# Kernel tuning notes

Hardware: AMD Instinct MI355X
Metric: run time of the kernel (lower is better)

The kernel has to match this reference:

```python
import jax, jax.numpy as jnp
import numpy as np

VOCAB, H, L, T = 50257, 1024, 2, 4096


def setup_inputs() -> dict:
    key = jax.random.key(0)
    ks = jax.random.split(key, 6)
    s = 1.0 / np.sqrt(H)  # torch GRU init scale
    return {
        "input_tensor": jax.random.randint(ks[0], (T,), 0, VOCAB, dtype=jnp.int64 if jax.config.jax_enable_x64 else jnp.int32),
        "embeddings": jax.random.normal(ks[1], (VOCAB, H), dtype=jnp.float32),
        "w_ih": jax.random.uniform(ks[2], (L, 3 * H, H), jnp.float32, -s, s),
        "w_hh": jax.random.uniform(ks[3], (L, 3 * H, H), jnp.float32, -s, s),
        "b_ih": jax.random.uniform(ks[4], (L, 3 * H), jnp.float32, -s, s),
        "b_hh": jax.random.uniform(ks[5], (L, 3 * H), jnp.float32, -s, s),
    }


def _gru_layer(x, wih, whh, bih, bhh):
    # x: [T, H]; returns outputs [T, H] and final hidden [H]
    gi = x @ wih.T + bih  # [T, 3H], input projections precomputed

    def step(h, gi_t):
        gh = h @ whh.T + bhh  # [3H]
        i_r, i_z, i_n = jnp.split(gi_t, 3)
        h_r, h_z, h_n = jnp.split(gh, 3)
        r = jax.nn.sigmoid(i_r + h_r)
        z = jax.nn.sigmoid(i_z + h_z)
        n = jnp.tanh(i_n + r * h_n)
        h_new = (1.0 - z) * n + z * h
        return h_new, h_new

    h0 = jnp.zeros((x.shape[-1],), x.dtype)
    h_fin, ys = jax.lax.scan(step, h0, gi)
    return ys, h_fin


def reference(input_tensor, embeddings, w_ih, w_hh, b_ih, b_hh):
    x = embeddings[input_tensor]  # [T, H] embedding lookup
    finals = []
    for l in range(w_ih.shape[0]):  # small fixed layer count
        x, h_fin = _gru_layer(x, w_ih[l], w_hh[l], b_ih[l], b_hh[l])
        finals.append(h_fin)
    encoder_outputs = x  # [T, H]
    encoder_hidden = jnp.stack(finals)[:, None, :]  # [L, 1, H]
    return encoder_outputs, encoder_hidden
```

## Files before the change

### kernel.cpp

```cpp
#include <hip/hip_runtime.h>
#include <hip/hip_bf16.h>


#define TT    4096
#define HDIM  1024
#define L0WG  64
#define L1WG  128
#define SBS   512
#define NREP  8
typedef unsigned long long u64;

__global__ void embed_kernel(const int* __restrict__ idx,
                             const float* __restrict__ emb,
                             float* __restrict__ x) {
    int t = blockIdx.x;
    int row = idx[t];
    const float4* src = reinterpret_cast<const float4*>(emb + (size_t)row * HDIM);
    float4* dst = reinterpret_cast<float4*>(x + (size_t)t * HDIM);
    dst[threadIdx.x] = src[threadIdx.x];
}

#define BM 64
#define BN 64
#define BK 32
__global__ __launch_bounds__(256)
void gemm_nt_bias(const float* __restrict__ A,
                  const float* __restrict__ Bw,
                  const float* __restrict__ bias,
                  float* __restrict__ C,
                  int M, int N, int K) {
    __shared__ float As[BK][BM];
    __shared__ float Bs[BK][BN];
    const int tid = threadIdx.x;
    const int m0 = blockIdx.x * BM;
    const int n0 = blockIdx.y * BN;
    const int tx = tid & 15, ty = tid >> 4;
    const int lr = tid >> 3;
    const int lc = (tid & 7) * 4;

    float acc[4][4] = {};

    for (int k0 = 0; k0 < K; k0 += BK) {
#pragma unroll
        for (int pass = 0; pass < 2; ++pass) {
            int m = lr + pass * 32;
            float4 v = *reinterpret_cast<const float4*>(A + (size_t)(m0 + m) * K + k0 + lc);
            As[lc + 0][m] = v.x; As[lc + 1][m] = v.y;
            As[lc + 2][m] = v.z; As[lc + 3][m] = v.w;
            float4 u = *reinterpret_cast<const float4*>(Bw + (size_t)(n0 + m) * K + k0 + lc);
            Bs[lc + 0][m] = u.x; Bs[lc + 1][m] = u.y;
            Bs[lc + 2][m] = u.z; Bs[lc + 3][m] = u.w;
        }
        __syncthreads();
#pragma unroll
        for (int kk = 0; kk < BK; ++kk) {
            float4 a = *reinterpret_cast<const float4*>(&As[kk][ty * 4]);
            float4 b = *reinterpret_cast<const float4*>(&Bs[kk][tx * 4]);
            float av[4] = {a.x, a.y, a.z, a.w};
            float bv[4] = {b.x, b.y, b.z, b.w};
#pragma unroll
            for (int i = 0; i < 4; ++i)
#pragma unroll
                for (int j = 0; j < 4; ++j)
                    acc[i][j] = fmaf(av[i], bv[j], acc[i][j]);
        }
        __syncthreads();
    }

    float4 b4 = *reinterpret_cast<const float4*>(bias + n0 + tx * 4);
    float bb[4] = {b4.x, b4.y, b4.z, b4.w};
#pragma unroll
    for (int i = 0; i < 4; ++i) {
        int m = m0 + ty * 4 + i;
        float4 o;
        o.x = acc[i][0] + bb[0];
        o.y = acc[i][1] + bb[1];
        o.z = acc[i][2] + bb[2];
        o.w = acc[i][3] + bb[3];
        *reinterpret_cast<float4*>(C + (size_t)m * N + n0 + tx * 4) = o;
    }
}

__device__ __forceinline__ float dot4(float4 a, float4 b) {
    return fmaf(a.x, b.x, fmaf(a.y, b.y, fmaf(a.z, b.z, a.w * b.w)));
}
__device__ __forceinline__ float fsig(float x) { return 1.f / (1.f + __expf(-x)); }
__device__ __forceinline__ float ftanh(float x) {
    return fmaf(-2.f, 1.f / (1.f + __expf(2.f * x)), 1.f);
}
__device__ __forceinline__ u64 pack_h(unsigned seq, float h) {
    return ((u64)seq << 32) | (u64)__float_as_uint(h);
}
__device__ __forceinline__ u64 aload(const u64* p) {
    return __hip_atomic_load(p, __ATOMIC_RELAXED, __HIP_MEMORY_SCOPE_AGENT);
}
__device__ __forceinline__ u64 poll_h(const u64* p, unsigned need) {
    u64 v = aload(p);
    while ((unsigned)(v >> 32) < need) v = aload(p);
    return v;
}
__device__ __forceinline__ void poll2(const u64* p0, const u64* p1, unsigned need,
                                      u64& v0, u64& v1) {
    v0 = aload(p0);
    v1 = aload(p1);
    while ((unsigned)(v0 >> 32) < need || (unsigned)(v1 >> 32) < need) {
        v0 = aload(p0);
        v1 = aload(p1);
    }
}
__device__ __forceinline__ void pub_h(u64* rep, int par, int idx, u64 v) {
#pragma unroll
    for (int r = 0; r < NREP; ++r)
        __hip_atomic_store(rep + ((size_t)r * 2 + par) * HDIM + idx, v,
                           __ATOMIC_RELAXED, __HIP_MEMORY_SCOPE_AGENT);
}
__device__ __forceinline__ void stage_y(const u64* lrow, unsigned need,
                                        float* lds_y, int l) {
    u64 v[16];
#pragma unroll
    for (int k = 0; k < 16; ++k) v[k] = aload(lrow + k * 64 + l);
#pragma unroll
    for (int k = 0; k < 16; ++k)
        while ((unsigned)(v[k] >> 32) < need) v[k] = aload(lrow + k * 64 + l);
#pragma unroll
    for (int k = 0; k < 16; ++k)
        lds_y[k * 64 + l] = __uint_as_float((unsigned)v[k]);
}

__global__ __launch_bounds__(SBS, 1)
void gru_pipe(const float* __restrict__ gi0,
              const float* __restrict__ whh0,
              const float* __restrict__ bhh0,
              const float* __restrict__ wih1,
              const float* __restrict__ whh1,
              const float* __restrict__ bih1,
              const float* __restrict__ bhh1,
              u64* y0log,
              float* __restrict__ out,
              u64* h0rep, u64* h1rep) {
    const int tid  = threadIdx.x;
    const int slot = tid >> 3;
    const int l8   = tid & 7;
    const int xcd  = blockIdx.x & 7;

    __shared__ float lds_h[HDIM];
    __shared__ float lds_y[HDIM];
    __shared__ float lds_gh[48];

    if (blockIdx.x < L0WG) {
        const int g = blockIdx.x;

        float4 Wlo[16], Whi[16];
        if (slot < 48) {
            const int q = slot >> 4, jl = slot & 15;
            const float4* row4 = reinterpret_cast<const float4*>(
                whh0 + (size_t)(q * HDIM + g * 16 + jl) * HDIM);
#pragma unroll
            for (int k4 = 0; k4 < 16; ++k4) Wlo[k4] = row4[k4 * 8 + l8];
#pragma unroll
            for (int k4 = 0; k4 < 16; ++k4) Whi[k4] = row4[(k4 + 16) * 8 + l8];
        } else {
#pragma unroll
            for (int k4 = 0; k4 < 16; ++k4) { Wlo[k4] = float4{0,0,0,0}; Whi[k4] = float4{0,0,0,0}; }
        }

        float bh0 = 0.f, bh1 = 0.f, bh2 = 0.f;
        float gir = 0.f, giz = 0.f, gin = 0.f;
        float h_own = 0.f;
        if (tid < 16) {
            const int gj = g * 16 + tid;
            bh0 = bhh0[0 * HDIM + gj];
            bh1 = bhh0[1 * HDIM + gj];
            bh2 = bhh0[2 * HDIM + gj];
            gir = gi0[gj];
            giz = gi0[HDIM + gj];
            gin = gi0[2 * HDIM + gj];
        }

        lds_h[tid] = 0.f;
        lds_h[tid + SBS] = 0.f;
        __syncthreads();

        const float4* lh4 = reinterpret_cast<const float4*>(lds_h);

        for (int t = 0; t < TT; ++t) {
            float nir = 0.f, niz = 0.f, nin = 0.f;
            if (tid < 16 && t + 1 < TT) {
                const float* base = gi0 + (size_t)(t + 1) * 3 * HDIM + g * 16 + tid;
                nir = base[0];
                niz = base[HDIM];
                nin = base[2 * HDIM];
            }

            if (slot < 48) {
                float p0 = 0.f, p1 = 0.f;
#pragma unroll
                for (int k4 = 0; k4 < 16; ++k4) p0 += dot4(Wlo[k4], lh4[k4 * 8 + l8]);
#pragma unroll
                for (int k4 = 0; k4 < 16; ++k4) p1 += dot4(Whi[k4], lh4[(k4 + 16) * 8 + l8]);
                float p = p0 + p1;
                p += __shfl_xor(p, 1);
                p += __shfl_xor(p, 2);
                p += __shfl_xor(p, 4);
                if (l8 == 0) lds_gh[slot] = p;
            }
            __syncthreads();

            if (tid < 16) {
                const int gj = g * 16 + tid;
                const float hr = lds_gh[tid]      + bh0;
                const float hz = lds_gh[16 + tid] + bh1;
                const float hn = lds_gh[32 + tid] + bh2;
                const float r = fsig(gir + hr);
                const float z = fsig(giz + hz);
                const float n = ftanh(gin + r * hn);
                const float h_new = (1.f - z) * n + z * h_own;
                h_own = h_new;
                const u64 pk = pack_h((unsigned)(t + 1), h_new);
                pub_h(h0rep, (t + 1) & 1, gj, pk);
                __hip_atomic_store(y0log + (size_t)t * HDIM + gj, pk,
                                   __ATOMIC_RELAXED, __HIP_MEMORY_SCOPE_AGENT);
                if (t == TT - 1) out[(size_t)TT * HDIM + gj] = h_new;
            }

            {
                const unsigned need = (unsigned)(t + 1);
                const u64* hp = h0rep + ((size_t)xcd * 2 + ((t + 1) & 1)) * HDIM;
                u64 v0, v1;
                poll2(hp + 2 * tid, hp + 2 * tid + 1, need, v0, v1);
                float2 hv;
                hv.x = __uint_as_float((unsigned)v0);
                hv.y = __uint_as_float((unsigned)v1);
                reinterpret_cast<float2*>(lds_h)[tid] = hv;
            }
            gir = nir; giz = niz; gin = nin;
            __syncthreads();
        }
    } else {
        const int g1 = blockIdx.x - L0WG;

        float4 Wlo[16], Whi[16];
        if (slot < 48) {
            const int ss = (slot < 24) ? slot : slot - 24;
            const int q = ss >> 3, jl = ss & 7;
            const float* mat = (slot < 24) ? whh1 : wih1;
            const float4* row4 = reinterpret_cast<const float4*>(
                mat + (size_t)(q * HDIM + g1 * 8 + jl) * HDIM);
#pragma unroll
            for (int k4 = 0; k4 < 16; ++k4) Wlo[k4] = row4[k4 * 8 + l8];
#pragma unroll
            for (int k4 = 0; k4 < 16; ++k4) Whi[k4] = row4[(k4 + 16) * 8 + l8];
        } else {
#pragma unroll
            for (int k4 = 0; k4 < 16; ++k4) { Wlo[k4] = float4{0,0,0,0}; Whi[k4] = float4{0,0,0,0}; }
        }

        float bh0 = 0.f, bh1 = 0.f, bh2 = 0.f;
        float bi0 = 0.f, bi1 = 0.f, bi2 = 0.f;
        float h_own = 0.f;
        if (tid < 8) {
            const int u = g1 * 8 + tid;
            bh0 = bhh1[0 * HDIM + u];
            bh1 = bhh1[1 * HDIM + u];
            bh2 = bhh1[2 * HDIM + u];
            bi0 = bih1[0 * HDIM + u];
            bi1 = bih1[1 * HDIM + u];
            bi2 = bih1[2 * HDIM + u];
        }

        lds_h[tid] = 0.f;
        lds_h[tid + SBS] = 0.f;
        if (tid >= 448) {
            stage_y(y0log, 1u, lds_y, tid - 448);
        }
        __syncthreads();

        const float4* lh4 = reinterpret_cast<const float4*>(lds_h);
        const float4* ly4 = reinterpret_cast<const float4*>(lds_y);

        for (int t = 0; t < TT; ++t) {
            if (slot < 48) {
                const float4* s4 = (slot < 24) ? lh4 : ly4;
                float p0 = 0.f, p1 = 0.f;
#pragma unroll
                for (int k4 = 0; k4 < 16; ++k4) p0 += dot4(Wlo[k4], s4[k4 * 8 + l8]);
#pragma unroll
                for (int k4 = 0; k4 < 16; ++k4) p1 += dot4(Whi[k4], s4[(k4 + 16) * 8 + l8]);
                float p = p0 + p1;
                p += __shfl_xor(p, 1);
                p += __shfl_xor(p, 2);
                p += __shfl_xor(p, 4);
                if (l8 == 0) lds_gh[slot] = p;
            }
            __syncthreads();

            if (tid < 8) {
                const int u = g1 * 8 + tid;
                const float hr = lds_gh[tid]      + bh0;
                const float hz = lds_gh[8 + tid]  + bh1;
                const float hn = lds_gh[16 + tid] + bh2;
                const float ir = lds_gh[24 + tid] + bi0;
                const float iz = lds_gh[32 + tid] + bi1;
                const float in_ = lds_gh[40 + tid] + bi2;
                const float r = fsig(ir + hr);
                const float z = fsig(iz + hz);
                const float n = ftanh(in_ + r * hn);
                const float h_new = (1.f - z) * n + z * h_own;
                h_own = h_new;
                pub_h(h1rep, (t + 1) & 1, u, pack_h((unsigned)(t + 1), h_new));
                out[(size_t)t * HDIM + u] = h_new;
                if (t == TT - 1) out[(size_t)TT * HDIM + HDIM + u] = h_new;
            }

            if (tid >= 448 && t + 1 < TT) {
                stage_y(y0log + (size_t)(t + 1) * HDIM, (unsigned)(t + 2),
                        lds_y, tid - 448);
            }

            {
                const unsigned need = (unsigned)(t + 1);
                const u64* hp = h1rep + ((size_t)xcd * 2 + ((t + 1) & 1)) * HDIM;
                u64 v0, v1;
                poll2(hp + 2 * tid, hp + 2 * tid + 1, need, v0, v1);
                float2 hv;
                hv.x = __uint_as_float((unsigned)v0);
                hv.y = __uint_as_float((unsigned)v1);
                reinterpret_cast<float2*>(lds_h)[tid] = hv;
            }
            __syncthreads();
        }
    }
}

extern "C" void kernel_launch(void* const* d_in, const int* in_sizes, int n_in,
                              void* d_out, int out_size, void* d_ws, size_t ws_size,
                              hipStream_t stream) {
    const int*   idx = (const int*)d_in[0];
    const float* emb = (const float*)d_in[1];
    const float* wih = (const float*)d_in[2];
    const float* whh = (const float*)d_in[3];
    const float* bih = (const float*)d_in[4];
    const float* bhh = (const float*)d_in[5];
    float* out = (float*)d_out;

    float* x     = (float*)d_ws;
    float* gi    = x  + (size_t)TT * HDIM;
    u64*   y0log = (u64*)(gi + (size_t)TT * 3 * HDIM);
    u64*   h0rep = y0log + (size_t)TT * HDIM;
    u64*   h1rep = h0rep + (size_t)NREP * 2 * HDIM;
    size_t zero_bytes = ((size_t)TT * HDIM + 2 * (size_t)NREP * 2 * HDIM) * 8;

    hipMemsetAsync(y0log, 0, zero_bytes, stream);

    embed_kernel<<<TT, 256, 0, stream>>>(idx, emb, x);

    const size_t wstride = (size_t)3 * HDIM * HDIM;
    const size_t bstride = (size_t)3 * HDIM;

    gemm_nt_bias<<<dim3(TT / BM, 3 * HDIM / BN), 256, 0, stream>>>(
        x, wih, bih, gi, TT, 3 * HDIM, HDIM);

    gru_pipe<<<L0WG + L1WG, SBS, 0, stream>>>(
        gi, whh, bhh,
        wih + wstride, whh + wstride, bih + bstride, bhh + bstride,
        y0log, out, h0rep, h1rep);
}
```

Baseline: 10.10 ms.

## Halve layer-1 workgroups, stage W_ih1 in LDS as bf16, prefetch y0 ahead

Layer 1 now runs on 64 workgroups of 16 hidden units each instead of 128 of 8. W_hh1 stays in registers, while this block's W_ih1 rows are converted to bf16 and kept in LDS. The input projection for step t+1 is computed from a double-buffered y0 row during the wait for the recurrent h broadcast, and waves 6-7 prefetch y0 two steps ahead. The intent is to shrink the set of participants in the per-step h1 exchange and take the input GEMV off the critical path. In exchange it adds bf16 rounding error on the input weights, about 96KB of LDS use, and a startup wait until layer 0 is LAG steps ahead.

```diff
diff --git a/kernel.cpp b/kernel.cpp
--- a/kernel.cpp
+++ b/kernel.cpp
@@ -5,9 +5,11 @@
 #define TT    4096
 #define HDIM  1024
 #define L0WG  64
-#define L1WG  128
+#define L1WG  64
 #define SBS   512
 #define NREP  8
+#define LAG   8
+typedef unsigned short ushort_t;
 typedef unsigned long long u64;
 
 __global__ void embed_kernel(const int* __restrict__ idx,
@@ -88,6 +90,12 @@
 __device__ __forceinline__ float ftanh(float x) {
     return fmaf(-2.f, 1.f / (1.f + __expf(2.f * x)), 1.f);
 }
+__device__ __forceinline__ float bflo(unsigned u) { return __uint_as_float(u << 16); }
+__device__ __forceinline__ float bfhi(unsigned u) { return __uint_as_float(u & 0xffff0000u); }
+__device__ __forceinline__ ushort_t f2bf(float f) {
+    unsigned u = __float_as_uint(f);
+    return (ushort_t)((u + 0x7FFFu + ((u >> 16) & 1u)) >> 16);
+}
 __device__ __forceinline__ u64 pack_h(unsigned seq, float h) {
     return ((u64)seq << 32) | (u64)__float_as_uint(h);
 }
@@ -114,17 +122,18 @@
         __hip_atomic_store(rep + ((size_t)r * 2 + par) * HDIM + idx, v,
                            __ATOMIC_RELAXED, __HIP_MEMORY_SCOPE_AGENT);
 }
-__device__ __forceinline__ void stage_y(const u64* lrow, unsigned need,
-                                        float* lds_y, int l) {
-    u64 v[16];
-#pragma unroll
-    for (int k = 0; k < 16; ++k) v[k] = aload(lrow + k * 64 + l);
-#pragma unroll
-    for (int k = 0; k < 16; ++k)
-        while ((unsigned)(v[k] >> 32) < need) v[k] = aload(lrow + k * 64 + l);
-#pragma unroll
-    for (int k = 0; k < 16; ++k)
-        lds_y[k * 64 + l] = __uint_as_float((unsigned)v[k]);
+__device__ __forceinline__ float dot_bf16(uint2 w0, uint2 w1, uint2 w2, uint2 w3,
+                                          float4 yA, float4 yB, float4 yC, float4 yD) {
+    float p = 0.f;
+    p = fmaf(bflo(w0.x), yA.x, p); p = fmaf(bfhi(w0.x), yA.y, p);
+    p = fmaf(bflo(w0.y), yA.z, p); p = fmaf(bfhi(w0.y), yA.w, p);
+    p = fmaf(bflo(w1.x), yB.x, p); p = fmaf(bfhi(w1.x), yB.y, p);
+    p = fmaf(bflo(w1.y), yB.z, p); p = fmaf(bfhi(w1.y), yB.w, p);
+    p = fmaf(bflo(w2.x), yC.x, p); p = fmaf(bfhi(w2.x), yC.y, p);
+    p = fmaf(bflo(w2.y), yC.z, p); p = fmaf(bfhi(w2.y), yC.w, p);
+    p = fmaf(bflo(w3.x), yD.x, p); p = fmaf(bfhi(w3.x), yD.y, p);
+    p = fmaf(bflo(w3.y), yD.z, p); p = fmaf(bfhi(w3.y), yD.w, p);
+    return p;
 }
 
 __global__ __launch_bounds__(SBS, 1)
@@ -141,11 +150,15 @@
     const int tid  = threadIdx.x;
     const int slot = tid >> 3;
     const int l8   = tid & 7;
+    const int wv   = tid >> 6;
+    const int ln   = tid & 63;
     const int xcd  = blockIdx.x & 7;
 
-    __shared__ float lds_h[HDIM];
-    __shared__ float lds_y[HDIM];
+    __shared__ __align__(16) ushort_t lds_wi[48 * HDIM];
+    __shared__ __align__(16) float lds_h[HDIM];
+    __shared__ __align__(16) float lds_y[2][HDIM];
     __shared__ float lds_gh[48];
+    __shared__ float lds_gi[2][48];
 
     if (blockIdx.x < L0WG) {
         const int g = blockIdx.x;
@@ -238,14 +251,13 @@
         }
     } else {
         const int g1 = blockIdx.x - L0WG;
+        const int u0 = g1 * 16;
 
         float4 Wlo[16], Whi[16];
         if (slot < 48) {
-            const int ss = (slot < 24) ? slot : slot - 24;
-            const int q = ss >> 3, jl = ss & 7;
-            const float* mat = (slot < 24) ? whh1 : wih1;
+            const int q = slot >> 4, jl = slot & 15;
             const float4* row4 = reinterpret_cast<const float4*>(
-                mat + (size_t)(q * HDIM + g1 * 8 + jl) * HDIM);
+                whh1 + (size_t)(q * HDIM + u0 + jl) * HDIM);
 #pragma unroll
             for (int k4 = 0; k4 < 16; ++k4) Wlo[k4] = row4[k4 * 8 + l8];
 #pragma unroll
@@ -255,56 +267,95 @@
             for (int k4 = 0; k4 < 16; ++k4) { Wlo[k4] = float4{0,0,0,0}; Whi[k4] = float4{0,0,0,0}; }
         }
 
-        float bh0 = 0.f, bh1 = 0.f, bh2 = 0.f;
-        float bi0 = 0.f, bi1 = 0.f, bi2 = 0.f;
+        for (int i = tid; i < 48 * 512; i += SBS) {
+            const int r = i >> 9, c = i & 511;
+            const size_t grow = (size_t)((r >> 4) * HDIM + u0 + (r & 15)) * HDIM;
+            const float2 a = *reinterpret_cast<const float2*>(wih1 + grow + 2 * c);
+            reinterpret_cast<unsigned*>(lds_wi)[r * 512 + c] =
+                (unsigned)f2bf(a.x) | ((unsigned)f2bf(a.y) << 16);
+        }
+
+        float bir = 0.f, biz = 0.f, bin = 0.f;
+        float bhr = 0.f, bhz = 0.f, bhn = 0.f;
         float h_own = 0.f;
-        if (tid < 8) {
-            const int u = g1 * 8 + tid;
-            bh0 = bhh1[0 * HDIM + u];
-            bh1 = bhh1[1 * HDIM + u];
-            bh2 = bhh1[2 * HDIM + u];
-            bi0 = bih1[0 * HDIM + u];
-            bi1 = bih1[1 * HDIM + u];
-            bi2 = bih1[2 * HDIM + u];
+        if (tid < 16) {
+            const int u = u0 + tid;
+            bir = bih1[u]; biz = bih1[HDIM + u]; bin = bih1[2 * HDIM + u];
+            bhr = bhh1[u]; bhz = bhh1[HDIM + u]; bhn = bhh1[2 * HDIM + u];
         }
 
         lds_h[tid] = 0.f;
         lds_h[tid + SBS] = 0.f;
-        if (tid >= 448) {
-            stage_y(y0log, 1u, lds_y, tid - 448);
+
+        if (tid == 0) (void)poll_h(y0log + (size_t)(LAG - 1) * HDIM, (unsigned)LAG);
+        __syncthreads();
+
+#pragma unroll
+        for (int s = 0; s < 2; ++s)
+#pragma unroll
+            for (int k = 0; k < 2; ++k) {
+                u64 v = poll_h(y0log + (size_t)s * HDIM + k * 512 + tid, (unsigned)(s + 1));
+                lds_y[s][k * 512 + tid] = __uint_as_float((unsigned)v);
+            }
+        __syncthreads();
+
+        if (wv < 6) {
+            const float4* ly4 = reinterpret_cast<const float4*>(lds_y[0]);
+            float4 yA = ly4[ln], yB = ly4[64 + ln], yC = ly4[128 + ln], yD = ly4[192 + ln];
+            const uint2* wi2 = reinterpret_cast<const uint2*>(lds_wi);
+#pragma unroll
+            for (int rr = 0; rr < 8; ++rr) {
+                const int row = wv * 8 + rr;
+                const uint2* wr = wi2 + row * 256;
+                float p = dot_bf16(wr[ln], wr[64 + ln], wr[128 + ln], wr[192 + ln],
+                                   yA, yB, yC, yD);
+                p += __shfl_xor(p, 1);  p += __shfl_xor(p, 2);
+                p += __shfl_xor(p, 4);  p += __shfl_xor(p, 8);
+                p += __shfl_xor(p, 16); p += __shfl_xor(p, 32);
+                if (ln == 0) lds_gi[0][row] = p;
+            }
         }
         __syncthreads();
 
         const float4* lh4 = reinterpret_cast<const float4*>(lds_h);
-        const float4* ly4 = reinterpret_cast<const float4*>(lds_y);
 
         for (int t = 0; t < TT; ++t) {
             if (slot < 48) {
-                const float4* s4 = (slot < 24) ? lh4 : ly4;
                 float p0 = 0.f, p1 = 0.f;
 #pragma unroll
-                for (int k4 = 0; k4 < 16; ++k4) p0 += dot4(Wlo[k4], s4[k4 * 8 + l8]);
-#pragma unroll
-                for (int k4 = 0; k4 < 16; ++k4) p1 += dot4(Whi[k4], s4[(k4 + 16) * 8 + l8]);
+                for (int k4 = 0; k4 < 16; ++k4) p0 += dot4(Wlo[k4], lh4[k4 * 8 + l8]);
+#pragma unroll
+                for (int k4 = 0; k4 < 16; ++k4) p1 += dot4(Whi[k4], lh4[(k4 + 16) * 8 + l8]);
                 float p = p0 + p1;
                 p += __shfl_xor(p, 1);
                 p += __shfl_xor(p, 2);
                 p += __shfl_xor(p, 4);
                 if (l8 == 0) lds_gh[slot] = p;
+            } else if (wv >= 6) {
+                const int s = t + 2;
+                if (s < TT) {
+                    const int tl = tid - 384;
+                    const u64* lr = y0log + (size_t)s * HDIM;
+                    u64 v[8];
+#pragma unroll
+                    for (int k = 0; k < 8; ++k) v[k] = aload(lr + k * 128 + tl);
+#pragma unroll
+                    for (int k = 0; k < 8; ++k)
+                        while ((unsigned)(v[k] >> 32) < (unsigned)(s + 1))
+                            v[k] = aload(lr + k * 128 + tl);
+#pragma unroll
+                    for (int k = 0; k < 8; ++k)
+                        lds_y[s & 1][k * 128 + tl] = __uint_as_float((unsigned)v[k]);
+                }
             }
             __syncthreads();
 
-            if (tid < 8) {
-                const int u = g1 * 8 + tid;
-                const float hr = lds_gh[tid]      + bh0;
-                const float hz = lds_gh[8 + tid]  + bh1;
-                const float hn = lds_gh[16 + tid] + bh2;
-                const float ir = lds_gh[24 + tid] + bi0;
-                const float iz = lds_gh[32 + tid] + bi1;
-                const float in_ = lds_gh[40 + tid] + bi2;
-                const float r = fsig(ir + hr);
-                const float z = fsig(iz + hz);
-                const float n = ftanh(in_ + r * hn);
+            if (tid < 16) {
+                const int u = u0 + tid;
+                const float r = fsig(lds_gi[t & 1][tid]      + bir + lds_gh[tid]      + bhr);
+                const float z = fsig(lds_gi[t & 1][16 + tid] + biz + lds_gh[16 + tid] + bhz);
+                const float n = ftanh(lds_gi[t & 1][32 + tid] + bin
+                                      + r * (lds_gh[32 + tid] + bhn));
                 const float h_new = (1.f - z) * n + z * h_own;
                 h_own = h_new;
                 pub_h(h1rep, (t + 1) & 1, u, pack_h((unsigned)(t + 1), h_new));
@@ -312,12 +363,24 @@
                 if (t == TT - 1) out[(size_t)TT * HDIM + HDIM + u] = h_new;
             }
 
-            if (tid >= 448 && t + 1 < TT) {
-                stage_y(y0log + (size_t)(t + 1) * HDIM, (unsigned)(t + 2),
-                        lds_y, tid - 448);
-            }
-
-            {
+            if (wv < 6 && t + 1 < TT) {
+                const float4* ly4 = reinterpret_cast<const float4*>(lds_y[(t + 1) & 1]);
+                float4 yA = ly4[ln], yB = ly4[64 + ln], yC = ly4[128 + ln], yD = ly4[192 + ln];
+                const uint2* wi2 = reinterpret_cast<const uint2*>(lds_wi);
+#pragma unroll
+                for (int rr = 0; rr < 8; ++rr) {
+                    const int row = wv * 8 + rr;
+                    const uint2* wr = wi2 + row * 256;
+                    float p = dot_bf16(wr[ln], wr[64 + ln], wr[128 + ln], wr[192 + ln],
+                                       yA, yB, yC, yD);
+                    p += __shfl_xor(p, 1);  p += __shfl_xor(p, 2);
+                    p += __shfl_xor(p, 4);  p += __shfl_xor(p, 8);
+                    p += __shfl_xor(p, 16); p += __shfl_xor(p, 32);
+                    if (ln == 0) lds_gi[(t + 1) & 1][row] = p;
+                }
+            }
+
+            if (t + 1 < TT) {
                 const unsigned need = (unsigned)(t + 1);
                 const u64* hp = h1rep + ((size_t)xcd * 2 + ((t + 1) & 1)) * HDIM;
                 u64 v0, v1;
```

New measurement: 16.34 ms. +61.8%, slower.

## Restructure GRU recurrence: per-wave row ownership, double-buffered LDS, one barrier per step

Applied to the files above, without the earlier changes.

Each wavefront (or half-wavefront in layer 0) now owns one hidden unit and computes all three gate dot products itself, reducing them with xor shuffles. This removes the LDS gate-partial exchange and one of the two block barriers per timestep. The h and y staging buffers are double-buffered so the single remaining barrier is enough. All threads now poll layer-0 outputs together with the layer-1 hidden state, replacing the dedicated staging waves. Publishing threads raise wave priority around the stores. The trade-off is more shuffle work and higher register pressure for the weight fragments held in every wave.

```diff
diff --git a/kernel.cpp b/kernel.cpp
--- a/kernel.cpp
+++ b/kernel.cpp
@@ -94,11 +94,6 @@
 __device__ __forceinline__ u64 aload(const u64* p) {
     return __hip_atomic_load(p, __ATOMIC_RELAXED, __HIP_MEMORY_SCOPE_AGENT);
 }
-__device__ __forceinline__ u64 poll_h(const u64* p, unsigned need) {
-    u64 v = aload(p);
-    while ((unsigned)(v >> 32) < need) v = aload(p);
-    return v;
-}
 __device__ __forceinline__ void poll2(const u64* p0, const u64* p1, unsigned need,
                                       u64& v0, u64& v1) {
     v0 = aload(p0);
@@ -108,23 +103,20 @@
         v1 = aload(p1);
     }
 }
+__device__ __forceinline__ void poll4(const u64* p0, const u64* p1, unsigned needh,
+                                      const u64* p2, const u64* p3, unsigned needy,
+                                      u64& v0, u64& v1, u64& v2, u64& v3) {
+    v0 = aload(p0); v1 = aload(p1); v2 = aload(p2); v3 = aload(p3);
+    while ((unsigned)(v0 >> 32) < needh || (unsigned)(v1 >> 32) < needh ||
+           (unsigned)(v2 >> 32) < needy || (unsigned)(v3 >> 32) < needy) {
+        v0 = aload(p0); v1 = aload(p1); v2 = aload(p2); v3 = aload(p3);
+    }
+}
 __device__ __forceinline__ void pub_h(u64* rep, int par, int idx, u64 v) {
 #pragma unroll
     for (int r = 0; r < NREP; ++r)
         __hip_atomic_store(rep + ((size_t)r * 2 + par) * HDIM + idx, v,
                            __ATOMIC_RELAXED, __HIP_MEMORY_SCOPE_AGENT);
-}
-__device__ __forceinline__ void stage_y(const u64* lrow, unsigned need,
-                                        float* lds_y, int l) {
-    u64 v[16];
-#pragma unroll
-    for (int k = 0; k < 16; ++k) v[k] = aload(lrow + k * 64 + l);
-#pragma unroll
-    for (int k = 0; k < 16; ++k)
-        while ((unsigned)(v[k] >> 32) < need) v[k] = aload(lrow + k * 64 + l);
-#pragma unroll
-    for (int k = 0; k < 16; ++k)
-        lds_y[k * 64 + l] = __uint_as_float((unsigned)v[k]);
 }
 
 __global__ __launch_bounds__(SBS, 1)
@@ -138,92 +130,76 @@
               u64* y0log,
               float* __restrict__ out,
               u64* h0rep, u64* h1rep) {
-    const int tid  = threadIdx.x;
-    const int slot = tid >> 3;
-    const int l8   = tid & 7;
-    const int xcd  = blockIdx.x & 7;
-
-    __shared__ float lds_h[HDIM];
-    __shared__ float lds_y[HDIM];
-    __shared__ float lds_gh[48];
+    const int tid = threadIdx.x;
+    const int xcd = blockIdx.x & 7;
+
+    __shared__ __align__(16) float lds_h[2][HDIM];
+    __shared__ __align__(16) float lds_y[2][HDIM];
 
     if (blockIdx.x < L0WG) {
         const int g = blockIdx.x;
-
-        float4 Wlo[16], Whi[16];
-        if (slot < 48) {
-            const int q = slot >> 4, jl = slot & 15;
-            const float4* row4 = reinterpret_cast<const float4*>(
-                whh0 + (size_t)(q * HDIM + g * 16 + jl) * HDIM);
-#pragma unroll
-            for (int k4 = 0; k4 < 16; ++k4) Wlo[k4] = row4[k4 * 8 + l8];
-#pragma unroll
-            for (int k4 = 0; k4 < 16; ++k4) Whi[k4] = row4[(k4 + 16) * 8 + l8];
-        } else {
-#pragma unroll
-            for (int k4 = 0; k4 < 16; ++k4) { Wlo[k4] = float4{0,0,0,0}; Whi[k4] = float4{0,0,0,0}; }
+        const int l = tid & 31;
+        const int u = g * 16 + (tid >> 5);
+
+        const float4* r0 = reinterpret_cast<const float4*>(whh0 + (size_t)(0 * HDIM + u) * HDIM);
+        const float4* r1 = reinterpret_cast<const float4*>(whh0 + (size_t)(1 * HDIM + u) * HDIM);
+        const float4* r2 = reinterpret_cast<const float4*>(whh0 + (size_t)(2 * HDIM + u) * HDIM);
+        float4 W0[8], W1[8], W2[8];
+#pragma unroll
+        for (int m = 0; m < 8; ++m) {
+            W0[m] = r0[m * 32 + l];
+            W1[m] = r1[m * 32 + l];
+            W2[m] = r2[m * 32 + l];
         }
 
         float bh0 = 0.f, bh1 = 0.f, bh2 = 0.f;
         float gir = 0.f, giz = 0.f, gin = 0.f;
         float h_own = 0.f;
-        if (tid < 16) {
-            const int gj = g * 16 + tid;
-            bh0 = bhh0[0 * HDIM + gj];
-            bh1 = bhh0[1 * HDIM + gj];
-            bh2 = bhh0[2 * HDIM + gj];
-            gir = gi0[gj];
-            giz = gi0[HDIM + gj];
-            gin = gi0[2 * HDIM + gj];
-        }
-
-        lds_h[tid] = 0.f;
-        lds_h[tid + SBS] = 0.f;
+        if (l == 0) {
+            bh0 = bhh0[u]; bh1 = bhh0[HDIM + u]; bh2 = bhh0[2 * HDIM + u];
+            gir = gi0[u];  giz = gi0[HDIM + u];  gin = gi0[2 * HDIM + u];
+        }
+
+        reinterpret_cast<float2*>(lds_h[0])[tid] = float2{0.f, 0.f};
         __syncthreads();
 
-        const float4* lh4 = reinterpret_cast<const float4*>(lds_h);
-
         for (int t = 0; t < TT; ++t) {
-            float nir = 0.f, niz = 0.f, nin = 0.f;
-            if (tid < 16 && t + 1 < TT) {
-                const float* base = gi0 + (size_t)(t + 1) * 3 * HDIM + g * 16 + tid;
-                nir = base[0];
-                niz = base[HDIM];
-                nin = base[2 * HDIM];
-            }
-
-            if (slot < 48) {
-                float p0 = 0.f, p1 = 0.f;
-#pragma unroll
-                for (int k4 = 0; k4 < 16; ++k4) p0 += dot4(Wlo[k4], lh4[k4 * 8 + l8]);
-#pragma unroll
-                for (int k4 = 0; k4 < 16; ++k4) p1 += dot4(Whi[k4], lh4[(k4 + 16) * 8 + l8]);
-                float p = p0 + p1;
-                p += __shfl_xor(p, 1);
-                p += __shfl_xor(p, 2);
-                p += __shfl_xor(p, 4);
-                if (l8 == 0) lds_gh[slot] = p;
-            }
-            __syncthreads();
-
-            if (tid < 16) {
-                const int gj = g * 16 + tid;
-                const float hr = lds_gh[tid]      + bh0;
-                const float hz = lds_gh[16 + tid] + bh1;
-                const float hn = lds_gh[32 + tid] + bh2;
-                const float r = fsig(gir + hr);
-                const float z = fsig(giz + hz);
-                const float n = ftanh(gin + r * hn);
+            const float4* lh4 = reinterpret_cast<const float4*>(lds_h[t & 1]);
+            float p0 = 0.f, p1 = 0.f, p2 = 0.f;
+#pragma unroll
+            for (int m = 0; m < 8; ++m) {
+                const float4 h4 = lh4[m * 32 + l];
+                p0 += dot4(W0[m], h4);
+                p1 += dot4(W1[m], h4);
+                p2 += dot4(W2[m], h4);
+            }
+#pragma unroll
+            for (int o = 1; o < 32; o <<= 1) {
+                p0 += __shfl_xor(p0, o);
+                p1 += __shfl_xor(p1, o);
+                p2 += __shfl_xor(p2, o);
+            }
+
+            if (l == 0) {
+                __builtin_amdgcn_s_setprio(1);
+                const float r = fsig(gir + p0 + bh0);
+                const float z = fsig(giz + p1 + bh1);
+                const float n = ftanh(gin + r * (p2 + bh2));
                 const float h_new = (1.f - z) * n + z * h_own;
                 h_own = h_new;
                 const u64 pk = pack_h((unsigned)(t + 1), h_new);
-                pub_h(h0rep, (t + 1) & 1, gj, pk);
-                __hip_atomic_store(y0log + (size_t)t * HDIM + gj, pk,
+                pub_h(h0rep, (t + 1) & 1, u, pk);
+                __hip_atomic_store(y0log + (size_t)t * HDIM + u, pk,
                                    __ATOMIC_RELAXED, __HIP_MEMORY_SCOPE_AGENT);
-                if (t == TT - 1) out[(size_t)TT * HDIM + gj] = h_new;
-            }
-
-            {
+                __builtin_amdgcn_s_setprio(0);
+                if (t == TT - 1) out[(size_t)TT * HDIM + u] = h_new;
+                if (t + 1 < TT) {
+                    const float* b = gi0 + (size_t)(t + 1) * 3 * HDIM + u;
+                    gir = b[0]; giz = b[HDIM]; gin = b[2 * HDIM];
+                }
+            }
+
+            if (t + 1 < TT) {
                 const unsigned need = (unsigned)(t + 1);
                 const u64* hp = h0rep + ((size_t)xcd * 2 + ((t + 1) & 1)) * HDIM;
                 u64 v0, v1;
@@ -231,101 +207,101 @@
                 float2 hv;
                 hv.x = __uint_as_float((unsigned)v0);
                 hv.y = __uint_as_float((unsigned)v1);
-                reinterpret_cast<float2*>(lds_h)[tid] = hv;
-            }
-            gir = nir; giz = niz; gin = nin;
+                reinterpret_cast<float2*>(lds_h[(t + 1) & 1])[tid] = hv;
+            }
             __syncthreads();
         }
     } else {
         const int g1 = blockIdx.x - L0WG;
-
-        float4 Wlo[16], Whi[16];
-        if (slot < 48) {
-            const int ss = (slot < 24) ? slot : slot - 24;
-            const int q = ss >> 3, jl = ss & 7;
-            const float* mat = (slot < 24) ? whh1 : wih1;
-            const float4* row4 = reinterpret_cast<const float4*>(
-                mat + (size_t)(q * HDIM + g1 * 8 + jl) * HDIM);
-#pragma unroll
-            for (int k4 = 0; k4 < 16; ++k4) Wlo[k4] = row4[k4 * 8 + l8];
-#pragma unroll
-            for (int k4 = 0; k4 < 16; ++k4) Whi[k4] = row4[(k4 + 16) * 8 + l8];
-        } else {
-#pragma unroll
-            for (int k4 = 0; k4 < 16; ++k4) { Wlo[k4] = float4{0,0,0,0}; Whi[k4] = float4{0,0,0,0}; }
+        const int l = tid & 63;
+        const int u = g1 * 8 + (tid >> 6);
+
+        const float4* rh0 = reinterpret_cast<const float4*>(whh1 + (size_t)(0 * HDIM + u) * HDIM);
+        const float4* rh1 = reinterpret_cast<const float4*>(whh1 + (size_t)(1 * HDIM + u) * HDIM);
+        const float4* rh2 = reinterpret_cast<const float4*>(whh1 + (size_t)(2 * HDIM + u) * HDIM);
+        const float4* ri0 = reinterpret_cast<const float4*>(wih1 + (size_t)(0 * HDIM + u) * HDIM);
+        const float4* ri1 = reinterpret_cast<const float4*>(wih1 + (size_t)(1 * HDIM + u) * HDIM);
+        const float4* ri2 = reinterpret_cast<const float4*>(wih1 + (size_t)(2 * HDIM + u) * HDIM);
+        float4 WH0[4], WH1[4], WH2[4], WI0[4], WI1[4], WI2[4];
+#pragma unroll
+        for (int m = 0; m < 4; ++m) {
+            WH0[m] = rh0[m * 64 + l]; WH1[m] = rh1[m * 64 + l]; WH2[m] = rh2[m * 64 + l];
+            WI0[m] = ri0[m * 64 + l]; WI1[m] = ri1[m * 64 + l]; WI2[m] = ri2[m * 64 + l];
         }
 
         float bh0 = 0.f, bh1 = 0.f, bh2 = 0.f;
         float bi0 = 0.f, bi1 = 0.f, bi2 = 0.f;
         float h_own = 0.f;
-        if (tid < 8) {
-            const int u = g1 * 8 + tid;
-            bh0 = bhh1[0 * HDIM + u];
-            bh1 = bhh1[1 * HDIM + u];
-            bh2 = bhh1[2 * HDIM + u];
-            bi0 = bih1[0 * HDIM + u];
-            bi1 = bih1[1 * HDIM + u];
-            bi2 = bih1[2 * HDIM + u];
-        }
-
-        lds_h[tid] = 0.f;
-        lds_h[tid + SBS] = 0.f;
-        if (tid >= 448) {
-            stage_y(y0log, 1u, lds_y, tid - 448);
+        if (l == 0) {
+            bh0 = bhh1[u]; bh1 = bhh1[HDIM + u]; bh2 = bhh1[2 * HDIM + u];
+            bi0 = bih1[u]; bi1 = bih1[HDIM + u]; bi2 = bih1[2 * HDIM + u];
+        }
+
+        reinterpret_cast<float2*>(lds_h[0])[tid] = float2{0.f, 0.f};
+        {
+            u64 v0, v1;
+            poll2(y0log + 2 * tid, y0log + 2 * tid + 1, 1u, v0, v1);
+            float2 yv;
+            yv.x = __uint_as_float((unsigned)v0);
+            yv.y = __uint_as_float((unsigned)v1);
+            reinterpret_cast<float2*>(lds_y[0])[tid] = yv;
         }
         __syncthreads();
 
-        const float4* lh4 = reinterpret_cast<const float4*>(lds_h);
-        const float4* ly4 = reinterpret_cast<const float4*>(lds_y);
-
         for (int t = 0; t < TT; ++t) {
-            if (slot < 48) {
-                const float4* s4 = (slot < 24) ? lh4 : ly4;
-                float p0 = 0.f, p1 = 0.f;
-#pragma unroll
-                for (int k4 = 0; k4 < 16; ++k4) p0 += dot4(Wlo[k4], s4[k4 * 8 + l8]);
-#pragma unroll
-                for (int k4 = 0; k4 < 16; ++k4) p1 += dot4(Whi[k4], s4[(k4 + 16) * 8 + l8]);
-                float p = p0 + p1;
-                p += __shfl_xor(p, 1);
-                p += __shfl_xor(p, 2);
-                p += __shfl_xor(p, 4);
-                if (l8 == 0) lds_gh[slot] = p;
-            }
-            __syncthreads();
-
-            if (tid < 8) {
-                const int u = g1 * 8 + tid;
-                const float hr = lds_gh[tid]      + bh0;
-                const float hz = lds_gh[8 + tid]  + bh1;
-                const float hn = lds_gh[16 + tid] + bh2;
-                const float ir = lds_gh[24 + tid] + bi0;
-                const float iz = lds_gh[32 + tid] + bi1;
-                const float in_ = lds_gh[40 + tid] + bi2;
-                const float r = fsig(ir + hr);
-                const float z = fsig(iz + hz);
-                const float n = ftanh(in_ + r * hn);
+            const float4* lh4 = reinterpret_cast<const float4*>(lds_h[t & 1]);
+            const float4* ly4 = reinterpret_cast<const float4*>(lds_y[t & 1]);
+            float ph0 = 0.f, ph1 = 0.f, ph2 = 0.f;
+            float pi0 = 0.f, pi1 = 0.f, pi2 = 0.f;
+#pragma unroll
+            for (int m = 0; m < 4; ++m) {
+                const float4 h4 = lh4[m * 64 + l];
+                const float4 y4 = ly4[m * 64 + l];
+                ph0 += dot4(WH0[m], h4);
+                ph1 += dot4(WH1[m], h4);
+                ph2 += dot4(WH2[m], h4);
+                pi0 += dot4(WI0[m], y4);
+                pi1 += dot4(WI1[m], y4);
+                pi2 += dot4(WI2[m], y4);
+            }
+#pragma unroll
+            for (int o = 1; o < 64; o <<= 1) {
+                ph0 += __shfl_xor(ph0, o);
+                ph1 += __shfl_xor(ph1, o);
+                ph2 += __shfl_xor(ph2, o);
+                pi0 += __shfl_xor(pi0, o);
+                pi1 += __shfl_xor(pi1, o);
+                pi2 += __shfl_xor(pi2, o);
+            }
+
+            if (l == 0) {
+                __builtin_amdgcn_s_setprio(1);
+                const float r = fsig(pi0 + bi0 + ph0 + bh0);
+                const float z = fsig(pi1 + bi1 + ph1 + bh1);
+                const float n = ftanh(pi2 + bi2 + r * (ph2 + bh2));
                 const float h_new = (1.f - z) * n + z * h_own;
                 h_own = h_new;
                 pub_h(h1rep, (t + 1) & 1, u, pack_h((unsigned)(t + 1), h_new));
+                __builtin_amdgcn_s_setprio(0);
                 out[(size_t)t * HDIM + u] = h_new;
                 if (t == TT - 1) out[(size_t)TT * HDIM + HDIM + u] = h_new;
             }
 
-            if (tid >= 448 && t + 1 < TT) {
-                stage_y(y0log + (size_t)(t + 1) * HDIM, (unsigned)(t + 2),
-                        lds_y, tid - 448);
-            }
-
-            {
-                const unsigned need = (unsigned)(t + 1);
+            if (t + 1 < TT) {
+                const unsigned needh = (unsigned)(t + 1);
+                const unsigned needy = (unsigned)(t + 2);
                 const u64* hp = h1rep + ((size_t)xcd * 2 + ((t + 1) & 1)) * HDIM;
-                u64 v0, v1;
-                poll2(hp + 2 * tid, hp + 2 * tid + 1, need, v0, v1);
-                float2 hv;
+                const u64* yp = y0log + (size_t)(t + 1) * HDIM;
+                u64 v0, v1, v2, v3;
+                poll4(hp + 2 * tid, hp + 2 * tid + 1, needh,
+                      yp + 2 * tid, yp + 2 * tid + 1, needy, v0, v1, v2, v3);
+                float2 hv, yv;
                 hv.x = __uint_as_float((unsigned)v0);
                 hv.y = __uint_as_float((unsigned)v1);
-                reinterpret_cast<float2*>(lds_h)[tid] = hv;
+                yv.x = __uint_as_float((unsigned)v2);
+                yv.y = __uint_as_float((unsigned)v3);
+                reinterpret_cast<float2*>(lds_h[(t + 1) & 1])[tid] = hv;
+                reinterpret_cast<float2*>(lds_y[(t + 1) & 1])[tid] = yv;
             }
             __syncthreads();
         }
```

Measured after the change: 15.12 ms. +49.7%, slower.
